# Optimization experiments

Measured on AMD Instinct MI355X. Metric: run time of the kernel, lower is better.

## Reference

```python
import jax, jax.numpy as jnp
import numpy as np

N_NODES = 100000
N_EDGES = 3200000


def _gcn_norm(row, col, n):
    # GCNConv default: add self loops, sym norm D^-1/2 (A+I) D^-1/2
    loop = jnp.arange(n, dtype=row.dtype)
    r = jnp.concatenate([row, loop])
    c = jnp.concatenate([col, loop])
    deg = jax.ops.segment_sum(jnp.ones_like(r, dtype=jnp.float32), r, num_segments=n)
    dinv = jnp.where(deg > 0, jax.lax.rsqrt(deg), 0.0)
    norm = dinv[r] * dinv[c]  # [E+N]
    return r, c, norm


def _gcn_conv(x, W, b, r, c, norm, n):
    h = x @ W  # dense transform first (in > out)
    msg = h[c] * norm[:, None]  # gather sources, scale
    out = jax.ops.segment_sum(msg, r, num_segments=n)  # scatter to destinations
    return out + b


def setup_inputs() -> dict:
    key = jax.random.key(0)
    ks = jax.random.split(key, 5)
    x = jax.random.normal(ks[0], (N_NODES, 1433), dtype=jnp.float32)
    row = jax.random.randint(ks[1], (N_EDGES,), 0, N_NODES, dtype=jnp.int32)
    col = jax.random.randint(ks[2], (N_EDGES,), 0, N_NODES, dtype=jnp.int32)
    W1 = jax.random.normal(ks[3], (1433, 16), dtype=jnp.float32) * (1.0 / np.sqrt(1433))
    b1 = jnp.zeros((16,), dtype=jnp.float32)
    W2 = jax.random.normal(ks[4], (16, 7), dtype=jnp.float32) * (1.0 / np.sqrt(16))
    b2 = jnp.zeros((7,), dtype=jnp.float32)
    return {"x": x, "row": row, "col": col, "W1": W1, "b1": b1, "W2": W2, "b2": b2}


def reference(x, row, col, W1, b1, W2, b2):
    n = x.shape[0]
    r, c, norm = _gcn_norm(row, col, n)
    h = _gcn_conv(x, W1, b1, r, c, norm, n)
    h = jax.nn.relu(h)
    # dropout is identity in eval mode (reference is deterministic)
    h = _gcn_conv(h, W2, b2, r, c, norm, n)
    return jax.nn.log_softmax(h, axis=1)
```

## Files before the change

kernel.cpp:

```cpp
#include <hip/hip_runtime.h>
#include <math.h>

#define N_NODES 100000
#define N_EDGES 3200000
#define FIN     1433

__global__ void k_zero(int* __restrict__ p, int n) {
  int i = blockIdx.x * blockDim.x + threadIdx.x;
  if (i < n) p[i] = 0;
}

__global__ void k_hist(const int* __restrict__ row, int* __restrict__ cnt) {
  int e = blockIdx.x * blockDim.x + threadIdx.x;
  if (e < N_EDGES) atomicAdd(&cnt[row[e]], 1);
}

__global__ void k_dinv(const int* __restrict__ cnt, float* __restrict__ dinv) {
  int i = blockIdx.x * blockDim.x + threadIdx.x;
  if (i < N_NODES) dinv[i] = 1.0f / sqrtf((float)(cnt[i] + 1));
}

__global__ void k_scanA(const int* __restrict__ cnt, int* __restrict__ bsum) {
  __shared__ int sd[256];
  int t = threadIdx.x, b = blockIdx.x;
  int base = b * 1024 + t * 4;
  int s = 0;
#pragma unroll
  for (int m = 0; m < 4; m++) {
    int i = base + m;
    if (i < N_NODES) s += cnt[i];
  }
  sd[t] = s; __syncthreads();
  for (int off = 128; off > 0; off >>= 1) {
    if (t < off) sd[t] += sd[t + off];
    __syncthreads();
  }
  if (t == 0) bsum[b] = sd[0];
}

__global__ void k_scanB(int* __restrict__ bsum, int* __restrict__ rowStart, int nb) {
  __shared__ int sd[128];
  int t = threadIdx.x;
  int v = (t < nb) ? bsum[t] : 0;
  sd[t] = v;
  __syncthreads();
  for (int off = 1; off < 128; off <<= 1) {
    int add = (t >= off) ? sd[t - off] : 0;
    __syncthreads();
    sd[t] += add;
    __syncthreads();
  }
  if (t < nb) bsum[t] = (t == 0) ? 0 : sd[t - 1];
  if (t == 0) rowStart[N_NODES] = sd[nb - 1];
}

__global__ void k_scanC(const int* __restrict__ cnt, const int* __restrict__ bsum,
                        int* __restrict__ rowStart) {
  __shared__ int sd[256];
  int t = threadIdx.x, b = blockIdx.x;
  int base = b * 1024 + t * 4;
  int v[4], pre[4], s = 0;
#pragma unroll
  for (int m = 0; m < 4; m++) {
    int i = base + m;
    v[m] = (i < N_NODES) ? cnt[i] : 0;
    pre[m] = s; s += v[m];
  }
  sd[t] = s; __syncthreads();
  for (int off = 1; off < 256; off <<= 1) {
    int add = (t >= off) ? sd[t - off] : 0;
    __syncthreads();
    sd[t] += add;
    __syncthreads();
  }
  int ex = (t == 0) ? 0 : sd[t - 1];
  int base0 = bsum[b] + ex;
#pragma unroll
  for (int m = 0; m < 4; m++) {
    int i = base + m;
    if (i < N_NODES) rowStart[i] = base0 + pre[m];
  }
}

__global__ void k_scatter(const int* __restrict__ row, const int* __restrict__ col,
                          const int* __restrict__ rowStart, int* __restrict__ fill,
                          int* __restrict__ colc) {
  int e = blockIdx.x * blockDim.x + threadIdx.x;
  if (e < N_EDGES) {
    int r = row[e];
    int pos = rowStart[r] + atomicAdd(&fill[r], 1);
    colc[pos] = col[e];
  }
}

__global__ __launch_bounds__(64) void k_gemm1(const float* __restrict__ x,
                                              const float* __restrict__ W1,
                                              float* __restrict__ t1) {
  int rowi = blockIdx.x * 64 + threadIdx.x;
  if (rowi >= N_NODES) return;
  const float* __restrict__ xr = x + (size_t)rowi * FIN;

  float acc[16];
#pragma unroll
  for (int j = 0; j < 16; j++) acc[j] = 0.0f;

  float4 buf[8], nbuf[8];
#pragma unroll
  for (int m = 0; m < 8; m++) buf[m] = *(const float4*)(xr + m * 4);

  const int NCH = 44;
  for (int ch = 0; ch < NCH; ch++) {
    int kc = ch * 32;
    if (ch + 1 < NCH) {
#pragma unroll
      for (int m = 0; m < 8; m++) nbuf[m] = *(const float4*)(xr + kc + 32 + m * 4);
    }
#pragma unroll
    for (int m = 0; m < 8; m++) {
      float xv0 = buf[m].x, xv1 = buf[m].y, xv2 = buf[m].z, xv3 = buf[m].w;
      const float* w0 = &W1[(size_t)(kc + m * 4 + 0) * 16];
      const float* w1 = &W1[(size_t)(kc + m * 4 + 1) * 16];
      const float* w2 = &W1[(size_t)(kc + m * 4 + 2) * 16];
      const float* w3 = &W1[(size_t)(kc + m * 4 + 3) * 16];
#pragma unroll
      for (int j = 0; j < 16; j++) {
        acc[j] = fmaf(xv0, w0[j], acc[j]);
        acc[j] = fmaf(xv1, w1[j], acc[j]);
        acc[j] = fmaf(xv2, w2[j], acc[j]);
        acc[j] = fmaf(xv3, w3[j], acc[j]);
      }
    }
#pragma unroll
    for (int m = 0; m < 8; m++) buf[m] = nbuf[m];
  }
  for (int k = 1408; k < FIN; k++) {
    float xv = xr[k];
    const float* w = &W1[(size_t)k * 16];
#pragma unroll
    for (int j = 0; j < 16; j++) acc[j] = fmaf(xv, w[j], acc[j]);
  }

  float* o = t1 + (size_t)rowi * 16;
#pragma unroll
  for (int j = 0; j < 16; j += 4)
    *(float4*)(o + j) = make_float4(acc[j], acc[j + 1], acc[j + 2], acc[j + 3]);
}

__global__ __launch_bounds__(256) void k_agg1(const float* __restrict__ t1,
                                              const int* __restrict__ rowStart,
                                              const int* __restrict__ colc,
                                              const float* __restrict__ dinv,
                                              const float* __restrict__ b1,
                                              float* __restrict__ h1r) {
  int lane = threadIdx.x & 63;
  int wid  = threadIdx.x >> 6;
  int node = blockIdx.x * 4 + wid;
  if (node >= N_NODES) return;
  int q = lane & 3, slot = lane >> 2;
  int s0 = rowStart[node], s1 = rowStart[node + 1];
  float ax = 0.f, ay = 0.f, az = 0.f, aw = 0.f;
  for (int e = s0 + slot; e < s1; e += 16) {
    int c = colc[e];
    float w = dinv[c];
    float4 v = *(const float4*)(t1 + (size_t)c * 16 + q * 4);
    ax = fmaf(v.x, w, ax); ay = fmaf(v.y, w, ay);
    az = fmaf(v.z, w, az); aw = fmaf(v.w, w, aw);
  }
#pragma unroll
  for (int off = 4; off < 64; off <<= 1) {
    ax += __shfl_xor(ax, off, 64);
    ay += __shfl_xor(ay, off, 64);
    az += __shfl_xor(az, off, 64);
    aw += __shfl_xor(aw, off, 64);
  }
  float di = dinv[node];
  if (slot == 0) {
    float4 sv = *(const float4*)(t1 + (size_t)node * 16 + q * 4);
    float4 bb = *(const float4*)(b1 + q * 4);
    float4 o;
    o.x = fmaxf(0.f, di * (ax + di * sv.x) + bb.x);
    o.y = fmaxf(0.f, di * (ay + di * sv.y) + bb.y);
    o.z = fmaxf(0.f, di * (az + di * sv.z) + bb.z);
    o.w = fmaxf(0.f, di * (aw + di * sv.w) + bb.w);
    *(float4*)(h1r + (size_t)node * 16 + q * 4) = o;
  }
}

__global__ void k_gemm2(const float* __restrict__ h1r, const float* __restrict__ W2,
                        float* __restrict__ t2) {
  int i = blockIdx.x * blockDim.x + threadIdx.x;
  if (i >= N_NODES) return;
  float h[16];
#pragma unroll
  for (int k = 0; k < 16; k++) h[k] = h1r[(size_t)i * 16 + k];
  float a[7] = {0, 0, 0, 0, 0, 0, 0};
#pragma unroll
  for (int k = 0; k < 16; k++)
#pragma unroll
    for (int j = 0; j < 7; j++) a[j] = fmaf(h[k], W2[k * 7 + j], a[j]);
  float* o = t2 + (size_t)i * 8;
#pragma unroll
  for (int j = 0; j < 7; j++) o[j] = a[j];
  o[7] = 0.0f;
}

__global__ __launch_bounds__(256) void k_agg2(const float* __restrict__ t2,
                                              const int* __restrict__ rowStart,
                                              const int* __restrict__ colc,
                                              const float* __restrict__ dinv,
                                              const float* __restrict__ b2,
                                              float* __restrict__ out) {
  int lane = threadIdx.x & 63;
  int wid  = threadIdx.x >> 6;
  int node = blockIdx.x * 4 + wid;
  if (node >= N_NODES) return;
  int q = lane & 1, slot = lane >> 1;
  int s0 = rowStart[node], s1 = rowStart[node + 1];
  float ax = 0.f, ay = 0.f, az = 0.f, aw = 0.f;
  for (int e = s0 + slot; e < s1; e += 32) {
    int c = colc[e];
    float w = dinv[c];
    float4 v = *(const float4*)(t2 + (size_t)c * 8 + q * 4);
    ax = fmaf(v.x, w, ax); ay = fmaf(v.y, w, ay);
    az = fmaf(v.z, w, az); aw = fmaf(v.w, w, aw);
  }
#pragma unroll
  for (int off = 2; off < 64; off <<= 1) {
    ax += __shfl_xor(ax, off, 64);
    ay += __shfl_xor(ay, off, 64);
    az += __shfl_xor(az, off, 64);
    aw += __shfl_xor(aw, off, 64);
  }
  float di = dinv[node];
  float4 sv = *(const float4*)(t2 + (size_t)node * 8 + q * 4);
  float lg[4];
  float am[4] = {ax, ay, az, aw};
  float sm[4] = {sv.x, sv.y, sv.z, sv.w};
#pragma unroll
  for (int m = 0; m < 4; m++) {
    int j = 4 * q + m;
    float bb = (j < 7) ? b2[j] : 0.0f;
    lg[m] = di * (am[m] + di * sm[m]) + bb;
    if (j == 7) lg[m] = -1e30f;
  }
  float o4 = __shfl_xor(lg[0], 1, 64);
  float o5 = __shfl_xor(lg[1], 1, 64);
  float o6 = __shfl_xor(lg[2], 1, 64);
  if (lane == 0) {
    float a[7] = {lg[0], lg[1], lg[2], lg[3], o4, o5, o6};
    float mx = a[0];
#pragma unroll
    for (int j = 1; j < 7; j++) mx = fmaxf(mx, a[j]);
    float s = 0.f;
#pragma unroll
    for (int j = 0; j < 7; j++) s += expf(a[j] - mx);
    float lse = mx + logf(s);
    float* o = out + (size_t)node * 7;
#pragma unroll
    for (int j = 0; j < 7; j++) o[j] = a[j] - lse;
  }
}

extern "C" void kernel_launch(void* const* d_in, const int* in_sizes, int n_in,
                              void* d_out, int out_size, void* d_ws, size_t ws_size,
                              hipStream_t stream) {
  const float* x   = (const float*)d_in[0];
  const int*   row = (const int*)d_in[1];
  const int*   col = (const int*)d_in[2];
  const float* W1  = (const float*)d_in[3];
  const float* b1  = (const float*)d_in[4];
  const float* W2  = (const float*)d_in[5];
  const float* b2  = (const float*)d_in[6];
  float* out = (float*)d_out;

  char* w = (char*)d_ws;
  auto alloc = [&](size_t bytes) {
    char* p = w;
    w += (bytes + 255) & ~(size_t)255;
    return p;
  };
  int*   cnt      = (int*)alloc((size_t)N_NODES * 4);
  int*   fill     = (int*)alloc((size_t)N_NODES * 4);
  int*   rowStart = (int*)alloc((size_t)(N_NODES + 1) * 4);
  int*   bsum     = (int*)alloc(128 * 4);
  float* dinv     = (float*)alloc((size_t)N_NODES * 4);
  int*   colc     = (int*)alloc((size_t)N_EDGES * 4);
  float* t1       = (float*)alloc((size_t)N_NODES * 16 * 4);
  float* h1r      = (float*)alloc((size_t)N_NODES * 16 * 4);
  float* t2       = (float*)alloc((size_t)N_NODES * 8 * 4);

  const int NB = (N_NODES + 1023) / 1024;

  k_zero<<<(N_NODES + 255) / 256, 256, 0, stream>>>(cnt, N_NODES);
  k_zero<<<(N_NODES + 255) / 256, 256, 0, stream>>>(fill, N_NODES);
  k_hist<<<(N_EDGES + 255) / 256, 256, 0, stream>>>(row, cnt);
  k_dinv<<<(N_NODES + 255) / 256, 256, 0, stream>>>(cnt, dinv);
  k_scanA<<<NB, 256, 0, stream>>>(cnt, bsum);
  k_scanB<<<1, 128, 0, stream>>>(bsum, rowStart, NB);
  k_scanC<<<NB, 256, 0, stream>>>(cnt, bsum, rowStart);
  k_scatter<<<(N_EDGES + 255) / 256, 256, 0, stream>>>(row, col, rowStart, fill, colc);
  k_gemm1<<<(N_NODES + 63) / 64, 64, 0, stream>>>(x, W1, t1);
  k_agg1<<<(N_NODES + 3) / 4, 256, 0, stream>>>(t1, rowStart, colc, dinv, b1, h1r);
  k_gemm2<<<(N_NODES + 255) / 256, 256, 0, stream>>>(h1r, W2, t2);
  k_agg2<<<(N_NODES + 3) / 4, 256, 0, stream>>>(t2, rowStart, colc, dinv, b2, out);
}
```

Measured before the change: 1.218 ms.

## Fuse preprocessing kernels, split GEMM1 K across waves, fold dinv and GEMM2 into aggregation

This bundles several changes. The histogram now reads rows as int4, dinv is computed inside scanA, and scanC initialises fill with rowStart so the scatter drops a zeroing kernel and an extra lookup. GEMM1 splits the K dimension across 4 waves per block and reduces the partial sums through shared memory, giving more parallelism for the memory-bound read of x. Source rows are prescaled by dinv, which removes the per-edge dinv gather in both aggregations. GEMM2 is fused into agg1 using lane shuffles, which removes the h1r round-trip and one launch.

```diff
diff --git a/kernel.cpp b/kernel.cpp
--- a/kernel.cpp
+++ b/kernel.cpp
@@ -11,24 +11,31 @@
 }
 
 __global__ void k_hist(const int* __restrict__ row, int* __restrict__ cnt) {
-  int e = blockIdx.x * blockDim.x + threadIdx.x;
-  if (e < N_EDGES) atomicAdd(&cnt[row[e]], 1);
-}
-
-__global__ void k_dinv(const int* __restrict__ cnt, float* __restrict__ dinv) {
-  int i = blockIdx.x * blockDim.x + threadIdx.x;
-  if (i < N_NODES) dinv[i] = 1.0f / sqrtf((float)(cnt[i] + 1));
-}
-
-__global__ void k_scanA(const int* __restrict__ cnt, int* __restrict__ bsum) {
+  int e4 = blockIdx.x * blockDim.x + threadIdx.x;
+  if (e4 * 4 < N_EDGES) {
+    int4 r = *(const int4*)(row + e4 * 4);
+    atomicAdd(&cnt[r.x], 1);
+    atomicAdd(&cnt[r.y], 1);
+    atomicAdd(&cnt[r.z], 1);
+    atomicAdd(&cnt[r.w], 1);
+  }
+}
+
+__global__ void k_scanA(const int* __restrict__ cnt, int* __restrict__ bsum,
+                        float* __restrict__ dinv) {
   __shared__ int sd[256];
   int t = threadIdx.x, b = blockIdx.x;
   int base = b * 1024 + t * 4;
   int s = 0;
-#pragma unroll
-  for (int m = 0; m < 4; m++) {
-    int i = base + m;
-    if (i < N_NODES) s += cnt[i];
+  if (base < N_NODES) {
+    int4 v = *(const int4*)(cnt + base);
+    s = v.x + v.y + v.z + v.w;
+    float4 d;
+    d.x = 1.0f / sqrtf((float)(v.x + 1));
+    d.y = 1.0f / sqrtf((float)(v.y + 1));
+    d.z = 1.0f / sqrtf((float)(v.z + 1));
+    d.w = 1.0f / sqrtf((float)(v.w + 1));
+    *(float4*)(dinv + base) = d;
   }
   sd[t] = s; __syncthreads();
   for (int off = 128; off > 0; off >>= 1) {
@@ -55,17 +62,13 @@
 }
 
 __global__ void k_scanC(const int* __restrict__ cnt, const int* __restrict__ bsum,
-                        int* __restrict__ rowStart) {
+                        int* __restrict__ rowStart, int* __restrict__ fill) {
   __shared__ int sd[256];
   int t = threadIdx.x, b = blockIdx.x;
   int base = b * 1024 + t * 4;
-  int v[4], pre[4], s = 0;
-#pragma unroll
-  for (int m = 0; m < 4; m++) {
-    int i = base + m;
-    v[m] = (i < N_NODES) ? cnt[i] : 0;
-    pre[m] = s; s += v[m];
-  }
+  int4 v = make_int4(0, 0, 0, 0);
+  if (base < N_NODES) v = *(const int4*)(cnt + base);
+  int s = v.x + v.y + v.z + v.w;
   sd[t] = s; __syncthreads();
   for (int off = 1; off < 256; off <<= 1) {
     int add = (t >= off) ? sd[t - off] : 0;
@@ -75,83 +78,110 @@
   }
   int ex = (t == 0) ? 0 : sd[t - 1];
   int base0 = bsum[b] + ex;
-#pragma unroll
-  for (int m = 0; m < 4; m++) {
-    int i = base + m;
-    if (i < N_NODES) rowStart[i] = base0 + pre[m];
+  if (base < N_NODES) {
+    int4 rs;
+    rs.x = base0;
+    rs.y = rs.x + v.x;
+    rs.z = rs.y + v.y;
+    rs.w = rs.z + v.z;
+    *(int4*)(rowStart + base) = rs;
+    *(int4*)(fill + base) = rs;
   }
 }
 
 __global__ void k_scatter(const int* __restrict__ row, const int* __restrict__ col,
-                          const int* __restrict__ rowStart, int* __restrict__ fill,
-                          int* __restrict__ colc) {
+                          int* __restrict__ fill, int* __restrict__ colc) {
   int e = blockIdx.x * blockDim.x + threadIdx.x;
   if (e < N_EDGES) {
-    int r = row[e];
-    int pos = rowStart[r] + atomicAdd(&fill[r], 1);
+    int pos = atomicAdd(&fill[row[e]], 1);
     colc[pos] = col[e];
   }
 }
 
-__global__ __launch_bounds__(64) void k_gemm1(const float* __restrict__ x,
-                                              const float* __restrict__ W1,
-                                              float* __restrict__ t1) {
-  int rowi = blockIdx.x * 64 + threadIdx.x;
-  if (rowi >= N_NODES) return;
-  const float* __restrict__ xr = x + (size_t)rowi * FIN;
+__global__ __launch_bounds__(256) void k_gemm1(const float* __restrict__ x,
+                                               const float* __restrict__ W1,
+                                               const float* __restrict__ dinv,
+                                               float* __restrict__ t1s) {
+  __shared__ float sd[4][64][16];
+  int lane = threadIdx.x & 63;
+  int wid  = threadIdx.x >> 6;
+  int rowi = blockIdx.x * 64 + lane;
 
   float acc[16];
 #pragma unroll
   for (int j = 0; j < 16; j++) acc[j] = 0.0f;
 
-  float4 buf[8], nbuf[8];
-#pragma unroll
-  for (int m = 0; m < 8; m++) buf[m] = *(const float4*)(xr + m * 4);
-
-  const int NCH = 44;
-  for (int ch = 0; ch < NCH; ch++) {
-    int kc = ch * 32;
-    if (ch + 1 < NCH) {
-#pragma unroll
-      for (int m = 0; m < 8; m++) nbuf[m] = *(const float4*)(xr + kc + 32 + m * 4);
-    }
-#pragma unroll
-    for (int m = 0; m < 8; m++) {
-      float xv0 = buf[m].x, xv1 = buf[m].y, xv2 = buf[m].z, xv3 = buf[m].w;
-      const float* w0 = &W1[(size_t)(kc + m * 4 + 0) * 16];
-      const float* w1 = &W1[(size_t)(kc + m * 4 + 1) * 16];
-      const float* w2 = &W1[(size_t)(kc + m * 4 + 2) * 16];
-      const float* w3 = &W1[(size_t)(kc + m * 4 + 3) * 16];
-#pragma unroll
-      for (int j = 0; j < 16; j++) {
-        acc[j] = fmaf(xv0, w0[j], acc[j]);
-        acc[j] = fmaf(xv1, w1[j], acc[j]);
-        acc[j] = fmaf(xv2, w2[j], acc[j]);
-        acc[j] = fmaf(xv3, w3[j], acc[j]);
+  if (rowi < N_NODES) {
+    const float* __restrict__ xr = x + (size_t)rowi * FIN;
+    float4 buf[8], nbuf[8];
+    {
+      const float* p = xr + wid * 32;
+#pragma unroll
+      for (int m = 0; m < 8; m++) buf[m] = *(const float4*)(p + m * 4);
+    }
+    for (int it = 0; it < 11; it++) {
+      int kc = (it * 4 + wid) * 32;
+      if (it < 10) {
+        const float* p = xr + kc + 128;
+#pragma unroll
+        for (int m = 0; m < 8; m++) nbuf[m] = *(const float4*)(p + m * 4);
       }
-    }
-#pragma unroll
-    for (int m = 0; m < 8; m++) buf[m] = nbuf[m];
-  }
-  for (int k = 1408; k < FIN; k++) {
-    float xv = xr[k];
-    const float* w = &W1[(size_t)k * 16];
-#pragma unroll
-    for (int j = 0; j < 16; j++) acc[j] = fmaf(xv, w[j], acc[j]);
-  }
-
-  float* o = t1 + (size_t)rowi * 16;
+#pragma unroll
+      for (int m = 0; m < 8; m++) {
+        float xv0 = buf[m].x, xv1 = buf[m].y, xv2 = buf[m].z, xv3 = buf[m].w;
+        const float* w0 = &W1[(size_t)(kc + m * 4 + 0) * 16];
+        const float* w1 = &W1[(size_t)(kc + m * 4 + 1) * 16];
+        const float* w2 = &W1[(size_t)(kc + m * 4 + 2) * 16];
+        const float* w3 = &W1[(size_t)(kc + m * 4 + 3) * 16];
+#pragma unroll
+        for (int j = 0; j < 16; j++) {
+          acc[j] = fmaf(xv0, w0[j], acc[j]);
+          acc[j] = fmaf(xv1, w1[j], acc[j]);
+          acc[j] = fmaf(xv2, w2[j], acc[j]);
+          acc[j] = fmaf(xv3, w3[j], acc[j]);
+        }
+      }
+#pragma unroll
+      for (int m = 0; m < 8; m++) buf[m] = nbuf[m];
+    }
+    if (wid == 3) {
+      for (int k = 1408; k < FIN; k++) {
+        float xv = xr[k];
+        const float* wv = &W1[(size_t)k * 16];
+#pragma unroll
+        for (int j = 0; j < 16; j++) acc[j] = fmaf(xv, wv[j], acc[j]);
+      }
+    }
+  }
+
 #pragma unroll
   for (int j = 0; j < 16; j += 4)
-    *(float4*)(o + j) = make_float4(acc[j], acc[j + 1], acc[j + 2], acc[j + 3]);
-}
-
-__global__ __launch_bounds__(256) void k_agg1(const float* __restrict__ t1,
+    *(float4*)(&sd[wid][lane][j]) = make_float4(acc[j], acc[j + 1], acc[j + 2], acc[j + 3]);
+  __syncthreads();
+
+  int r2 = blockIdx.x * 64 + lane;
+  if (r2 < N_NODES) {
+    float4 s0 = *(const float4*)(&sd[0][lane][wid * 4]);
+    float4 s1 = *(const float4*)(&sd[1][lane][wid * 4]);
+    float4 s2 = *(const float4*)(&sd[2][lane][wid * 4]);
+    float4 s3 = *(const float4*)(&sd[3][lane][wid * 4]);
+    float di = dinv[r2];
+    float4 o;
+    o.x = di * ((s0.x + s1.x) + (s2.x + s3.x));
+    o.y = di * ((s0.y + s1.y) + (s2.y + s3.y));
+    o.z = di * ((s0.z + s1.z) + (s2.z + s3.z));
+    o.w = di * ((s0.w + s1.w) + (s2.w + s3.w));
+    *(float4*)(t1s + (size_t)r2 * 16 + wid * 4) = o;
+  }
+}
+
+__global__ __launch_bounds__(256) void k_agg1(const float* __restrict__ t1s,
                                               const int* __restrict__ rowStart,
                                               const int* __restrict__ colc,
                                               const float* __restrict__ dinv,
                                               const float* __restrict__ b1,
-                                              float* __restrict__ h1r) {
+                                              const float* __restrict__ W2,
+                                              float* __restrict__ t2s) {
   int lane = threadIdx.x & 63;
   int wid  = threadIdx.x >> 6;
   int node = blockIdx.x * 4 + wid;
@@ -161,10 +191,8 @@
   float ax = 0.f, ay = 0.f, az = 0.f, aw = 0.f;
   for (int e = s0 + slot; e < s1; e += 16) {
     int c = colc[e];
-    float w = dinv[c];
-    float4 v = *(const float4*)(t1 + (size_t)c * 16 + q * 4);
-    ax = fmaf(v.x, w, ax); ay = fmaf(v.y, w, ay);
-    az = fmaf(v.z, w, az); aw = fmaf(v.w, w, aw);
+    float4 v = *(const float4*)(t1s + (size_t)c * 16 + q * 4);
+    ax += v.x; ay += v.y; az += v.z; aw += v.w;
   }
 #pragma unroll
   for (int off = 4; off < 64; off <<= 1) {
@@ -173,38 +201,35 @@
     az += __shfl_xor(az, off, 64);
     aw += __shfl_xor(aw, off, 64);
   }
-  float di = dinv[node];
   if (slot == 0) {
-    float4 sv = *(const float4*)(t1 + (size_t)node * 16 + q * 4);
+    float di = dinv[node];
+    float4 sv = *(const float4*)(t1s + (size_t)node * 16 + q * 4);
     float4 bb = *(const float4*)(b1 + q * 4);
-    float4 o;
-    o.x = fmaxf(0.f, di * (ax + di * sv.x) + bb.x);
-    o.y = fmaxf(0.f, di * (ay + di * sv.y) + bb.y);
-    o.z = fmaxf(0.f, di * (az + di * sv.z) + bb.z);
-    o.w = fmaxf(0.f, di * (aw + di * sv.w) + bb.w);
-    *(float4*)(h1r + (size_t)node * 16 + q * 4) = o;
-  }
-}
-
-__global__ void k_gemm2(const float* __restrict__ h1r, const float* __restrict__ W2,
-                        float* __restrict__ t2) {
-  int i = blockIdx.x * blockDim.x + threadIdx.x;
-  if (i >= N_NODES) return;
-  float h[16];
-#pragma unroll
-  for (int k = 0; k < 16; k++) h[k] = h1r[(size_t)i * 16 + k];
-  float a[7] = {0, 0, 0, 0, 0, 0, 0};
-#pragma unroll
-  for (int k = 0; k < 16; k++)
-#pragma unroll
-    for (int j = 0; j < 7; j++) a[j] = fmaf(h[k], W2[k * 7 + j], a[j]);
-  float* o = t2 + (size_t)i * 8;
-#pragma unroll
-  for (int j = 0; j < 7; j++) o[j] = a[j];
-  o[7] = 0.0f;
-}
-
-__global__ __launch_bounds__(256) void k_agg2(const float* __restrict__ t2,
+    float h0 = fmaxf(0.f, di * (ax + sv.x) + bb.x);
+    float h1 = fmaxf(0.f, di * (ay + sv.y) + bb.y);
+    float h2 = fmaxf(0.f, di * (az + sv.z) + bb.z);
+    float h3 = fmaxf(0.f, di * (aw + sv.w) + bb.w);
+    float p[8];
+#pragma unroll
+    for (int j = 0; j < 7; j++) {
+      const float* wr = W2 + (size_t)(4 * q) * 7 + j;
+      p[j] = h0 * wr[0] + h1 * wr[7] + h2 * wr[14] + h3 * wr[21];
+    }
+    p[7] = 0.f;
+#pragma unroll
+    for (int j = 0; j < 8; j++) {
+      p[j] += __shfl_xor(p[j], 1, 64);
+      p[j] += __shfl_xor(p[j], 2, 64);
+    }
+    if (q < 2) {
+      float4 o = make_float4(di * p[4 * q + 0], di * p[4 * q + 1],
+                             di * p[4 * q + 2], di * p[4 * q + 3]);
+      *(float4*)(t2s + (size_t)node * 8 + q * 4) = o;
+    }
+  }
+}
+
+__global__ __launch_bounds__(256) void k_agg2(const float* __restrict__ t2s,
                                               const int* __restrict__ rowStart,
                                               const int* __restrict__ colc,
                                               const float* __restrict__ dinv,
@@ -219,10 +244,8 @@
   float ax = 0.f, ay = 0.f, az = 0.f, aw = 0.f;
   for (int e = s0 + slot; e < s1; e += 32) {
     int c = colc[e];
-    float w = dinv[c];
-    float4 v = *(const float4*)(t2 + (size_t)c * 8 + q * 4);
-    ax = fmaf(v.x, w, ax); ay = fmaf(v.y, w, ay);
-    az = fmaf(v.z, w, az); aw = fmaf(v.w, w, aw);
+    float4 v = *(const float4*)(t2s + (size_t)c * 8 + q * 4);
+    ax += v.x; ay += v.y; az += v.z; aw += v.w;
   }
 #pragma unroll
   for (int off = 2; off < 64; off <<= 1) {
@@ -232,7 +255,7 @@
     aw += __shfl_xor(aw, off, 64);
   }
   float di = dinv[node];
-  float4 sv = *(const float4*)(t2 + (size_t)node * 8 + q * 4);
+  float4 sv = *(const float4*)(t2s + (size_t)node * 8 + q * 4);
   float lg[4];
   float am[4] = {ax, ay, az, aw};
   float sm[4] = {sv.x, sv.y, sv.z, sv.w};
@@ -240,7 +263,7 @@
   for (int m = 0; m < 4; m++) {
     int j = 4 * q + m;
     float bb = (j < 7) ? b2[j] : 0.0f;
-    lg[m] = di * (am[m] + di * sm[m]) + bb;
+    lg[m] = di * (am[m] + sm[m]) + bb;
     if (j == 7) lg[m] = -1e30f;
   }
   float o4 = __shfl_xor(lg[0], 1, 64);
@@ -285,22 +308,18 @@
   int*   bsum     = (int*)alloc(128 * 4);
   float* dinv     = (float*)alloc((size_t)N_NODES * 4);
   int*   colc     = (int*)alloc((size_t)N_EDGES * 4);
-  float* t1       = (float*)alloc((size_t)N_NODES * 16 * 4);
-  float* h1r      = (float*)alloc((size_t)N_NODES * 16 * 4);
-  float* t2       = (float*)alloc((size_t)N_NODES * 8 * 4);
+  float* t1s      = (float*)alloc((size_t)N_NODES * 16 * 4);
+  float* t2s      = (float*)alloc((size_t)N_NODES * 8 * 4);
 
   const int NB = (N_NODES + 1023) / 1024;
 
   k_zero<<<(N_NODES + 255) / 256, 256, 0, stream>>>(cnt, N_NODES);
-  k_zero<<<(N_NODES + 255) / 256, 256, 0, stream>>>(fill, N_NODES);
-  k_hist<<<(N_EDGES + 255) / 256, 256, 0, stream>>>(row, cnt);
-  k_dinv<<<(N_NODES + 255) / 256, 256, 0, stream>>>(cnt, dinv);
-  k_scanA<<<NB, 256, 0, stream>>>(cnt, bsum);
+  k_hist<<<(N_EDGES / 4 + 255) / 256, 256, 0, stream>>>(row, cnt);
+  k_scanA<<<NB, 256, 0, stream>>>(cnt, bsum, dinv);
   k_scanB<<<1, 128, 0, stream>>>(bsum, rowStart, NB);
-  k_scanC<<<NB, 256, 0, stream>>>(cnt, bsum, rowStart);
-  k_scatter<<<(N_EDGES + 255) / 256, 256, 0, stream>>>(row, col, rowStart, fill, colc);
-  k_gemm1<<<(N_NODES + 63) / 64, 64, 0, stream>>>(x, W1, t1);
-  k_agg1<<<(N_NODES + 3) / 4, 256, 0, stream>>>(t1, rowStart, colc, dinv, b1, h1r);
-  k_gemm2<<<(N_NODES + 255) / 256, 256, 0, stream>>>(h1r, W2, t2);
-  k_agg2<<<(N_NODES + 3) / 4, 256, 0, stream>>>(t2, rowStart, colc, dinv, b2, out);
-}
+  k_scanC<<<NB, 256, 0, stream>>>(cnt, bsum, rowStart, fill);
+  k_scatter<<<(N_EDGES + 255) / 256, 256, 0, stream>>>(row, col, fill, colc);
+  k_gemm1<<<(N_NODES + 63) / 64, 256, 0, stream>>>(x, W1, dinv, t1s);
+  k_agg1<<<(N_NODES + 3) / 4, 256, 0, stream>>>(t1s, rowStart, colc, dinv, b1, W2, t2s);
+  k_agg2<<<(N_NODES + 3) / 4, 256, 0, stream>>>(t2s, rowStart, colc, dinv, b2, out);
+}
```

Measured after the change: 1.643 ms. +34.8%, slower.
